# Optimization experiments

Hardware: AMD Instinct MI355X
Metric: run time of the kernel (lower is better)

Reference implementation:

```python
import jax, jax.numpy as jnp
import numpy as np

D, H = 256, 8
DH = D // H
NH, NL = 1024, 65536
EH, EL = 16384, 262144


def setup_inputs() -> dict:
    key = jax.random.key(0)
    ks = jax.random.split(key, 24)
    w = lambda i, s=0.05: jax.random.normal(ks[i], (D, D), jnp.float32) * s
    z = jnp.zeros((D,), jnp.float32)
    return {
        'high_emb_in': jax.random.normal(ks[0], (NH, D), jnp.float32),
        'low_emb_in': jax.random.normal(ks[1], (NL, D), jnp.float32),
        'high_edge_index': jax.random.randint(ks[2], (2, EH), 0, NH, jnp.int32),
        'low_edge_index': jax.random.randint(ks[3], (2, EL), 0, NL, jnp.int32),
        'low_batch': jnp.sort(jax.random.randint(ks[4], (NL,), 0, NH, jnp.int32)),
        'ln_g': jnp.ones((D,), jnp.float32), 'ln_b': z,
        'gin_eps': jnp.zeros((), jnp.float32), 'gin_w': w(5), 'gin_b': z,
        'mha_wq': w(6), 'mha_bq': z, 'mha_wk': w(7), 'mha_bk': z,
        'mha_wv': w(8), 'mha_bv': z, 'mha_wo': w(9), 'mha_bo': z,
        'tc_wq': w(10), 'tc_bq': z, 'tc_wk': w(11), 'tc_bk': z,
        'tc_wv': w(12), 'tc_bv': z, 'tc_wskip': w(13), 'tc_bskip': z,
        'chl_q': w(14), 'chl_k': w(15), 'chl_v': w(16),
        'clh_q': w(17), 'clh_k': w(18), 'clh_v': w(19),
    }


def _ln(x, g, b):
    m = x.mean(-1, keepdims=True)
    v = ((x - m) ** 2).mean(-1, keepdims=True)
    return (x - m) / jnp.sqrt(v + 1e-5) * g + b


def reference(high_emb_in, low_emb_in, ln_g, ln_b, gin_eps, gin_w, gin_b,
              mha_wq, mha_bq, mha_wk, mha_bk, mha_wv, mha_bv, mha_wo, mha_bo,
              tc_wq, tc_bq, tc_wk, tc_bk, tc_wv, tc_bv, tc_wskip, tc_bskip,
              chl_q, chl_k, chl_v, clh_q, clh_k, clh_v,
              high_edge_index, low_edge_index, low_batch):
    he = _ln(high_emb_in, ln_g, ln_b)
    le = _ln(low_emb_in, ln_g, ln_b)

    # --- GINConv(Linear) on high graph: Linear((1+eps)*x + sum_{j->i} x_j) ---
    hs, hd = high_edge_index[0], high_edge_index[1]
    agg = jax.ops.segment_sum(he[hs], hd, num_segments=NH)
    gin = ((1.0 + gin_eps) * he + agg) @ gin_w + gin_b

    # --- MultiheadAttention (unbatched self-attention over high nodes) ---
    q = (he @ mha_wq + mha_bq).reshape(NH, H, DH)
    k = (he @ mha_wk + mha_bk).reshape(NH, H, DH)
    v = (he @ mha_wv + mha_bv).reshape(NH, H, DH)
    logits = jnp.einsum('qhd,khd->hqk', q, k) * (1.0 / DH ** 0.5)
    attn = jax.nn.softmax(logits, axis=-1)
    mh = jnp.einsum('hqk,khd->qhd', attn, v).reshape(NH, D) @ mha_wo + mha_bo
    high = mh + gin

    # --- TransformerConv on low graph (concat heads + root skip) ---
    ls, lt = low_edge_index[0], low_edge_index[1]
    tq = (le @ tc_wq + tc_bq).reshape(NL, H, DH)
    tk = (le @ tc_wk + tc_bk).reshape(NL, H, DH)
    tv = (le @ tc_wv + tc_bv).reshape(NL, H, DH)
    lg = (tq[lt] * tk[ls]).sum(-1) * (1.0 / DH ** 0.5)  # [EL, H]
    mx = jax.ops.segment_max(lg, lt, num_segments=NL)
    p = jnp.exp(lg - mx[lt])
    den = jax.ops.segment_sum(p, lt, num_segments=NL)
    alpha = p / den[lt]
    msg = jax.ops.segment_sum(alpha[:, :, None] * tv[ls], lt, num_segments=NL)
    low = msg.reshape(NL, D) + le @ tc_wskip + tc_bskip

    # --- cross message passing ---
    cnt = jax.ops.segment_sum(jnp.ones((NL,), low.dtype), low_batch, num_segments=NH)
    xg = jax.ops.segment_sum(low, low_batch, num_segments=NH) / jnp.maximum(cnt, 1.0)[:, None]
    hpn = high[low_batch]
    sd = 1.0 / D ** 0.5
    w_hl = ((high @ chl_q) * (xg @ chl_k)).sum(1) * sd
    new_high = w_hl[:, None] * (high @ chl_v)
    w_lh = ((low @ clh_q) * (hpn @ clh_k)).sum(1) * sd
    new_low = w_lh[:, None] * (low @ clh_v)
    return (jax.nn.gelu(new_high, approximate=False),
            jax.nn.gelu(new_low, approximate=False))
```

## Files before the change

### kernel.cpp

```cpp
#include <hip/hip_runtime.h>
#include <math.h>

#define D 256
#define H 8
#define DH 32
#define NH 1024
#define NL 65536
#define EH 16384
#define EL 262144

typedef short bf16x8 __attribute__((ext_vector_type(8)));
typedef float f32x4 __attribute__((ext_vector_type(4)));

__device__ __forceinline__ float4 ld4(const float* p) { return *reinterpret_cast<const float4*>(p); }
__device__ __forceinline__ void st4(float* p, float4 v) { *reinterpret_cast<float4*>(p) = v; }
__device__ __forceinline__ float gelu_f(float x) { return 0.5f * x * (1.0f + erff(x * 0.70710678118654752f)); }
__device__ __forceinline__ ushort f2bf(float x) {
    union { float f; unsigned u; } v; v.f = x;
    unsigned r = v.u + 0x7FFF + ((v.u >> 16) & 1);
    return (ushort)(r >> 16);
}
__device__ __forceinline__ float bf2f(ushort u) {
    union { unsigned u; float f; } v; v.u = (unsigned)u << 16; return v.f;
}
__device__ __forceinline__ float4 bf4tof4(ushort4 u) {
    return make_float4(bf2f(u.x), bf2f(u.y), bf2f(u.z), bf2f(u.w));
}

__global__ __launch_bounds__(256) void ln_kernel(const float* __restrict__ hi, const float* __restrict__ lo,
                                                 const float* __restrict__ g, const float* __restrict__ b,
                                                 float* __restrict__ he, ushort* __restrict__ le16) {
    int row = blockIdx.x * 4 + (threadIdx.x >> 6);
    int lane = threadIdx.x & 63;
    const float* in = (row < NH) ? hi + (size_t)row * D : lo + (size_t)(row - NH) * D;
    float4 x = ld4(in + lane * 4);
    float s1 = x.x + x.y + x.z + x.w;
    float s2 = x.x * x.x + x.y * x.y + x.z * x.z + x.w * x.w;
    #pragma unroll
    for (int o = 32; o > 0; o >>= 1) { s1 += __shfl_xor(s1, o); s2 += __shfl_xor(s2, o); }
    float m = s1 * (1.0f / D);
    float var = s2 * (1.0f / D) - m * m;
    float rs = 1.0f / sqrtf(var + 1e-5f);
    float4 gg = ld4(g + lane * 4), bb = ld4(b + lane * 4);
    float4 y;
    y.x = (x.x - m) * rs * gg.x + bb.x;
    y.y = (x.y - m) * rs * gg.y + bb.y;
    y.z = (x.z - m) * rs * gg.z + bb.z;
    y.w = (x.w - m) * rs * gg.w + bb.w;
    if (row < NH) {
        st4(he + (size_t)row * D + lane * 4, y);
    } else {
        ushort4 u = make_ushort4(f2bf(y.x), f2bf(y.y), f2bf(y.z), f2bf(y.w));
        *reinterpret_cast<ushort4*>(le16 + (size_t)(row - NH) * D + lane * 4) = u;
    }
}

__global__ void concat_w(float* __restrict__ dst, const float* s0, const float* s1,
                         const float* s2, const float* s3, int nseg) {
    int total = 256 * nseg * 256;
    for (int idx = blockIdx.x * blockDim.x + threadIdx.x; idx < total; idx += gridDim.x * blockDim.x) {
        int ncol = nseg * 256;
        int r = idx / ncol, c = idx - r * ncol;
        int seg = c >> 8, cc = c & 255;
        const float* s = (seg == 0) ? s0 : (seg == 1) ? s1 : (seg == 2) ? s2 : s3;
        dst[idx] = s[r * 256 + cc];
    }
}
__global__ void concat_b(float* __restrict__ dst, const float* s0, const float* s1,
                         const float* s2, const float* s3, int nseg) {
    int idx = blockIdx.x * blockDim.x + threadIdx.x;
    if (idx < nseg * 256) {
        int seg = idx >> 8, cc = idx & 255;
        const float* s = (seg == 0) ? s0 : (seg == 1) ? s1 : (seg == 2) ? s2 : s3;
        dst[idx] = s[cc];
    }
}
__global__ __launch_bounds__(256) void concat_wT6(ushort* __restrict__ WlowT,
                                                  ushort* __restrict__ qT, ushort* __restrict__ vT,
                                                  const float* s18, const float* s20, const float* s22,
                                                  const float* s24, const float* s29, const float* s31) {
    int idx = blockIdx.x * 256 + threadIdx.x;
    int seg = idx >> 16, local = idx & 65535;
    int n = local >> 8, k = local & 255;
    const float* s; ushort* d; int off;
    switch (seg) {
        case 0: s = s18; d = WlowT; off = 0; break;
        case 1: s = s20; d = WlowT; off = 65536; break;
        case 2: s = s22; d = WlowT; off = 131072; break;
        case 3: s = s24; d = WlowT; off = 196608; break;
        case 4: s = s29; d = qT;    off = 0; break;
        default: s = s31; d = vT;   off = 0; break;
    }
    d[off + local] = f2bf(s[k * 256 + n]);
}

__global__ __launch_bounds__(256) void hcsr_count(const int* __restrict__ ei, int* __restrict__ counts) {
    int e = blockIdx.x * 256 + threadIdx.x;
    atomicAdd(&counts[ei[EH + e]], 1);
}
__global__ __launch_bounds__(256) void hscan(const int* __restrict__ cnt, int* __restrict__ rowptr) {
    __shared__ int s[256];
    int t = threadIdx.x;
    int v0 = cnt[t * 4], v1 = cnt[t * 4 + 1], v2 = cnt[t * 4 + 2], v3 = cnt[t * 4 + 3];
    int sum = v0 + v1 + v2 + v3;
    s[t] = sum;
    __syncthreads();
    for (int off = 1; off < 256; off <<= 1) {
        int v = (t >= off) ? s[t - off] : 0;
        __syncthreads();
        s[t] += v;
        __syncthreads();
    }
    int run = s[t] - sum;
    rowptr[t * 4] = run; run += v0;
    rowptr[t * 4 + 1] = run; run += v1;
    rowptr[t * 4 + 2] = run; run += v2;
    rowptr[t * 4 + 3] = run;
    if (t == 255) rowptr[NH] = EH;
}
__global__ __launch_bounds__(256) void hcsr_fill(const int* __restrict__ ei, const int* __restrict__ rowptr,
                                                 int* __restrict__ cursor, int* __restrict__ srcslot) {
    int e = blockIdx.x * 256 + threadIdx.x;
    int dst = ei[EH + e], src = ei[e];
    int pos = rowptr[dst] + atomicAdd(&cursor[dst], 1);
    srcslot[pos] = src;
}
__global__ __launch_bounds__(256) void gin_gather(const float* __restrict__ he, const int* __restrict__ rowptr,
                                                  const int* __restrict__ srcslot, const float* __restrict__ eps,
                                                  float* __restrict__ X) {
    int dst = blockIdx.x * 4 + (threadIdx.x >> 6);
    int lane = threadIdx.x & 63;
    float4 x = ld4(he + (size_t)dst * D + lane * 4);
    float e1 = 1.0f + eps[0];
    float4 acc = make_float4(e1 * x.x, e1 * x.y, e1 * x.z, e1 * x.w);
    int start = rowptr[dst], end = rowptr[dst + 1];
    for (int i = start; i < end; i++) {
        float4 v = ld4(he + (size_t)srcslot[i] * D + lane * 4);
        acc.x += v.x; acc.y += v.y; acc.z += v.z; acc.w += v.w;
    }
    st4(X + (size_t)dst * D + lane * 4, acc);
}

__global__ __launch_bounds__(256) void mm64(const float* __restrict__ A, int lda,
                                            const float* __restrict__ B, int ldb,
                                            const float* __restrict__ bias,
                                            const float* __restrict__ addC, int ldadd,
                                            float* __restrict__ C, int ldc) {
    __shared__ float As[16][64];
    __shared__ float Bs[16][64];
    int tid = threadIdx.x;
    int tx = tid & 15, ty = tid >> 4;
    int m0 = blockIdx.y * 64, n0 = blockIdx.x * 64;
    float acc[4][4];
    #pragma unroll
    for (int i = 0; i < 4; i++)
        #pragma unroll
        for (int j = 0; j < 4; j++) acc[i][j] = 0.0f;

    for (int k0 = 0; k0 < 256; k0 += 16) {
        {
            int row = tid >> 2, c4 = tid & 3;
            float4 a = ld4(A + (size_t)(m0 + row) * lda + k0 + c4 * 4);
            As[c4 * 4 + 0][row] = a.x; As[c4 * 4 + 1][row] = a.y;
            As[c4 * 4 + 2][row] = a.z; As[c4 * 4 + 3][row] = a.w;
        }
        {
            int row = tid >> 4, c4 = tid & 15;
            float4 b = ld4(B + (size_t)(k0 + row) * ldb + n0 + c4 * 4);
            st4(&Bs[row][c4 * 4], b);
        }
        __syncthreads();
        #pragma unroll
        for (int kk = 0; kk < 16; kk++) {
            float4 a4 = ld4(&As[kk][ty * 4]);
            float4 b4 = ld4(&Bs[kk][tx * 4]);
            float av[4] = {a4.x, a4.y, a4.z, a4.w};
            float bv[4] = {b4.x, b4.y, b4.z, b4.w};
            #pragma unroll
            for (int i = 0; i < 4; i++)
                #pragma unroll
                for (int j = 0; j < 4; j++) acc[i][j] += av[i] * bv[j];
        }
        __syncthreads();
    }
    float4 bj = bias ? ld4(bias + n0 + tx * 4) : make_float4(0.f, 0.f, 0.f, 0.f);
    #pragma unroll
    for (int i = 0; i < 4; i++) {
        size_t row = m0 + ty * 4 + i;
        float4 o = make_float4(acc[i][0] + bj.x, acc[i][1] + bj.y, acc[i][2] + bj.z, acc[i][3] + bj.w);
        if (addC) {
            float4 c = ld4(addC + row * ldadd + n0 + tx * 4);
            o.x += c.x; o.y += c.y; o.z += c.z; o.w += c.w;
        }
        st4(C + row * ldc + n0 + tx * 4, o);
    }
}

__global__ __launch_bounds__(256) void mm_bf16(const ushort* __restrict__ A, int lda,
                                               const ushort* __restrict__ BT,
                                               const float* __restrict__ bias,
                                               float* __restrict__ C, int ldc) {
    __shared__ ushort As[128][40];
    __shared__ ushort Bs[128][40];
    int tid = threadIdx.x;
    int lane = tid & 63, wave = tid >> 6;
    int wm = wave >> 1, wn = wave & 1;
    int m0 = blockIdx.y * 128, n0 = blockIdx.x * 128;
    int lrow = lane & 15, lgrp = lane >> 4;
    f32x4 acc[4][4];
    #pragma unroll
    for (int i = 0; i < 4; i++)
        #pragma unroll
        for (int j = 0; j < 4; j++) acc[i][j] = (f32x4){0.f, 0.f, 0.f, 0.f};

    int r0 = tid >> 2, q0 = tid & 3;
    int r1 = r0 + 64;
    for (int k0 = 0; k0 < 256; k0 += 32) {
        *(bf16x8*)&As[r0][q0 * 8] = *(const bf16x8*)&A[(size_t)(m0 + r0) * lda + k0 + q0 * 8];
        *(bf16x8*)&As[r1][q0 * 8] = *(const bf16x8*)&A[(size_t)(m0 + r1) * lda + k0 + q0 * 8];
        *(bf16x8*)&Bs[r0][q0 * 8] = *(const bf16x8*)&BT[(size_t)(n0 + r0) * 256 + k0 + q0 * 8];
        *(bf16x8*)&Bs[r1][q0 * 8] = *(const bf16x8*)&BT[(size_t)(n0 + r1) * 256 + k0 + q0 * 8];
        __syncthreads();
        bf16x8 af[4], bfr[4];
        #pragma unroll
        for (int f = 0; f < 4; f++) {
            af[f]  = *(const bf16x8*)&As[wm * 64 + f * 16 + lrow][lgrp * 8];
            bfr[f] = *(const bf16x8*)&Bs[wn * 64 + f * 16 + lrow][lgrp * 8];
        }
        #pragma unroll
        for (int i = 0; i < 4; i++)
            #pragma unroll
            for (int j = 0; j < 4; j++)
                acc[i][j] = __builtin_amdgcn_mfma_f32_16x16x32_bf16(af[i], bfr[j], acc[i][j], 0, 0, 0);
        __syncthreads();
    }
    #pragma unroll
    for (int i = 0; i < 4; i++) {
        #pragma unroll
        for (int j = 0; j < 4; j++) {
            int col = n0 + wn * 64 + j * 16 + lrow;
            float bb = bias ? bias[col] : 0.0f;
            #pragma unroll
            for (int r = 0; r < 4; r++) {
                int row = m0 + wm * 64 + i * 16 + lgrp * 4 + r;
                C[(size_t)row * ldc + col] = acc[i][j][r] + bb;
            }
        }
    }
}

__global__ __launch_bounds__(256) void mm_bf16_o16(const ushort* __restrict__ A, int lda,
                                                   const ushort* __restrict__ BT,
                                                   const float* __restrict__ bias,
                                                   ushort* __restrict__ C, int ldc) {
    __shared__ ushort As[128][40];
    __shared__ ushort Bs[128][40];
    int tid = threadIdx.x;
    int lane = tid & 63, wave = tid >> 6;
    int wm = wave >> 1, wn = wave & 1;
    int m0 = blockIdx.y * 128, n0 = blockIdx.x * 128;
    int lrow = lane & 15, lgrp = lane >> 4;
    f32x4 acc[4][4];
    #pragma unroll
    for (int i = 0; i < 4; i++)
        #pragma unroll
        for (int j = 0; j < 4; j++) acc[i][j] = (f32x4){0.f, 0.f, 0.f, 0.f};

    int r0 = tid >> 2, q0 = tid & 3;
    int r1 = r0 + 64;
    for (int k0 = 0; k0 < 256; k0 += 32) {
        *(bf16x8*)&As[r0][q0 * 8] = *(const bf16x8*)&A[(size_t)(m0 + r0) * lda + k0 + q0 * 8];
        *(bf16x8*)&As[r1][q0 * 8] = *(const bf16x8*)&A[(size_t)(m0 + r1) * lda + k0 + q0 * 8];
        *(bf16x8*)&Bs[r0][q0 * 8] = *(const bf16x8*)&BT[(size_t)(n0 + r0) * 256 + k0 + q0 * 8];
        *(bf16x8*)&Bs[r1][q0 * 8] = *(const bf16x8*)&BT[(size_t)(n0 + r1) * 256 + k0 + q0 * 8];
        __syncthreads();
        bf16x8 af[4], bfr[4];
        #pragma unroll
        for (int f = 0; f < 4; f++) {
            af[f]  = *(const bf16x8*)&As[wm * 64 + f * 16 + lrow][lgrp * 8];
            bfr[f] = *(const bf16x8*)&Bs[wn * 64 + f * 16 + lrow][lgrp * 8];
        }
        #pragma unroll
        for (int i = 0; i < 4; i++)
            #pragma unroll
            for (int j = 0; j < 4; j++)
                acc[i][j] = __builtin_amdgcn_mfma_f32_16x16x32_bf16(af[i], bfr[j], acc[i][j], 0, 0, 0);
        __syncthreads();
    }
    #pragma unroll
    for (int i = 0; i < 4; i++) {
        #pragma unroll
        for (int j = 0; j < 4; j++) {
            int col = n0 + wn * 64 + j * 16 + lrow;
            float bb = bias ? bias[col] : 0.0f;
            #pragma unroll
            for (int r = 0; r < 4; r++) {
                int row = m0 + wm * 64 + i * 16 + lgrp * 4 + r;
                C[(size_t)row * ldc + col] = f2bf(acc[i][j][r] + bb);
            }
        }
    }
}

__global__ __launch_bounds__(64) void attn_part(const float* __restrict__ qkv, float* __restrict__ part) {
    __shared__ float ks[64][32];
    __shared__ float vs[64][32];
    int h = blockIdx.y, kc = blockIdx.z;
    int q0 = blockIdx.x * 64;
    int t = threadIdx.x;
    float qr[32];
    const float* qp = qkv + (size_t)(q0 + t) * 768 + h * 32;
    #pragma unroll
    for (int d = 0; d < 32; d += 4) {
        float4 x = ld4(qp + d);
        qr[d] = x.x; qr[d + 1] = x.y; qr[d + 2] = x.z; qr[d + 3] = x.w;
    }
    int kt = kc * 64;
    #pragma unroll
    for (int j = 0; j < 8; j++) {
        int f = j * 64 + t;
        int row = f >> 3, c4 = f & 7;
        float4 kx = ld4(qkv + (size_t)(kt + row) * 768 + 256 + h * 32 + c4 * 4);
        st4(&ks[row][c4 * 4], kx);
        float4 vx = ld4(qkv + (size_t)(kt + row) * 768 + 512 + h * 32 + c4 * 4);
        st4(&vs[row][c4 * 4], vx);
    }
    __syncthreads();
    float l = 0.0f, acc[32];
    #pragma unroll
    for (int d = 0; d < 32; d++) acc[d] = 0.0f;
    const float scale = 0.17677669529663687f;
    #pragma unroll 4
    for (int kk = 0; kk < 64; kk++) {
        const float4* kr = reinterpret_cast<const float4*>(&ks[kk][0]);
        float s = 0.0f;
        #pragma unroll
        for (int d4 = 0; d4 < 8; d4++) {
            float4 kv = kr[d4];
            s += qr[d4*4]*kv.x + qr[d4*4+1]*kv.y + qr[d4*4+2]*kv.z + qr[d4*4+3]*kv.w;
        }
        float pe = __expf(s * scale);
        l += pe;
        const float4* vr = reinterpret_cast<const float4*>(&vs[kk][0]);
        #pragma unroll
        for (int d4 = 0; d4 < 8; d4++) {
            float4 vv = vr[d4];
            acc[d4*4] += pe*vv.x; acc[d4*4+1] += pe*vv.y; acc[d4*4+2] += pe*vv.z; acc[d4*4+3] += pe*vv.w;
        }
    }
    int q = q0 + t;
    size_t base = ((size_t)(h * 16 + kc) * 33) * 1024 + q;
    #pragma unroll
    for (int d = 0; d < 32; d++) part[base + (size_t)d * 1024] = acc[d];
    part[base + (size_t)32 * 1024] = l;
}

__global__ __launch_bounds__(64) void attn_combine(const float* __restrict__ part, float* __restrict__ out) {
    int h = blockIdx.y;
    int q = blockIdx.x * 64 + threadIdx.x;
    float acc[32], l = 0.0f;
    #pragma unroll
    for (int d = 0; d < 32; d++) acc[d] = 0.0f;
    for (int kc = 0; kc < 16; kc++) {
        size_t base = ((size_t)(h * 16 + kc) * 33) * 1024 + q;
        #pragma unroll
        for (int d = 0; d < 32; d++) acc[d] += part[base + (size_t)d * 1024];
        l += part[base + (size_t)32 * 1024];
    }
    float inv = 1.0f / l;
    float* op = out + (size_t)q * 256 + h * 32;
    #pragma unroll
    for (int d = 0; d < 32; d += 4)
        st4(op + d, make_float4(acc[d]*inv, acc[d+1]*inv, acc[d+2]*inv, acc[d+3]*inv));
}

__global__ __launch_bounds__(256) void csr_count(const int* __restrict__ ei, int* __restrict__ counts) {
    int e = blockIdx.x * 256 + threadIdx.x;
    atomicAdd(&counts[ei[EL + e]], 1);
}
__global__ __launch_bounds__(256) void scan_a(const int* __restrict__ counts, int* __restrict__ rowptr,
                                              int* __restrict__ bsum) {
    __shared__ int s[256];
    int t = threadIdx.x;
    int i = blockIdx.x * 256 + t;
    int c = counts[i];
    s[t] = c;
    __syncthreads();
    for (int off = 1; off < 256; off <<= 1) {
        int v = (t >= off) ? s[t - off] : 0;
        __syncthreads();
        s[t] += v;
        __syncthreads();
    }
    rowptr[i] = s[t] - c;
    if (t == 255) bsum[blockIdx.x] = s[255];
}
__global__ __launch_bounds__(256) void scan_b(int* __restrict__ bsum) {
    __shared__ int s[256];
    int t = threadIdx.x;
    int c = bsum[t];
    s[t] = c;
    __syncthreads();
    for (int off = 1; off < 256; off <<= 1) {
        int v = (t >= off) ? s[t - off] : 0;
        __syncthreads();
        s[t] += v;
        __syncthreads();
    }
    bsum[t] = s[t] - c;
}
__global__ __launch_bounds__(256) void scan_c(int* __restrict__ rowptr, const int* __restrict__ bsum) {
    int i = blockIdx.x * 256 + threadIdx.x;
    rowptr[i] += bsum[blockIdx.x];
    if (i == 0) rowptr[NL] = EL;
}
__global__ __launch_bounds__(256) void csr_fill(const int* __restrict__ ei, const int* __restrict__ rowptr,
                                                int* __restrict__ cursor, int* __restrict__ srcslot) {
    int e = blockIdx.x * 256 + threadIdx.x;
    int dst = ei[EL + e], src = ei[e];
    int pos = rowptr[dst] + atomicAdd(&cursor[dst], 1);
    srcslot[pos] = src;
}

__global__ __launch_bounds__(256) void edge_g1(const ushort* __restrict__ panel, const int* __restrict__ rowptr,
                                               const int* __restrict__ srcslot,
                                               float* __restrict__ p, float* __restrict__ den) {
    int dst = blockIdx.x * 4 + (threadIdx.x >> 6);
    int lane = threadIdx.x & 63, hh = lane >> 3;
    int start = rowptr[dst], end = rowptr[dst + 1];
    float4 q4 = bf4tof4(*(const ushort4*)&panel[(size_t)dst * 1024 + lane * 4]);
    float dl = 0.0f;
    for (int i = start; i < end; i++) {
        int src = srcslot[i];
        float4 k4 = bf4tof4(*(const ushort4*)&panel[(size_t)src * 1024 + 256 + lane * 4]);
        float s = q4.x * k4.x + q4.y * k4.y + q4.z * k4.z + q4.w * k4.w;
        s += __shfl_xor(s, 1); s += __shfl_xor(s, 2); s += __shfl_xor(s, 4);
        float pe = __expf(s * 0.17677669529663687f);
        dl += pe;
        if ((lane & 7) == 0) p[(size_t)i * 8 + hh] = pe;
    }
    if ((lane & 7) == 0) den[(size_t)dst * 8 + hh] = dl;
}

__global__ __launch_bounds__(256) void edge_g2(ushort* panel, const int* __restrict__ rowptr,
                                               const int* __restrict__ srcslot,
                                               const float* __restrict__ p, const float* __restrict__ den) {
    int dst = blockIdx.x * 4 + (threadIdx.x >> 6);
    int lane = threadIdx.x & 63, hh = lane >> 3;
    int start = rowptr[dst], end = rowptr[dst + 1];
    float dl = den[(size_t)dst * 8 + hh];
    float invd = (dl != 0.0f) ? 1.0f / dl : 0.0f;
    float4 acc = make_float4(0.f, 0.f, 0.f, 0.f);
    for (int i = start; i < end; i++) {
        int src = srcslot[i];
        float a = p[(size_t)i * 8 + hh] * invd;
        float4 v4 = bf4tof4(*(const ushort4*)&panel[(size_t)src * 1024 + 512 + lane * 4]);
        acc.x += a * v4.x; acc.y += a * v4.y; acc.z += a * v4.z; acc.w += a * v4.w;
    }
    ushort* op = panel + (size_t)dst * 1024 + 768 + lane * 4;
    float4 sk = bf4tof4(*(const ushort4*)op);
    ushort4 u = make_ushort4(f2bf(acc.x + sk.x), f2bf(acc.y + sk.y), f2bf(acc.z + sk.z), f2bf(acc.w + sk.w));
    *reinterpret_cast<ushort4*>(op) = u;
}

__global__ __launch_bounds__(256) void xg_kernel(const ushort* __restrict__ panel,
                                                 const int* __restrict__ batch, float* __restrict__ xg) {
    int i = blockIdx.x;
    int d = threadIdx.x;
    int lo = 0, hi = NL;
    while (lo < hi) { int mid = (lo + hi) >> 1; if (batch[mid] < i) lo = mid + 1; else hi = mid; }
    int start = lo;
    hi = NL;
    while (lo < hi) { int mid = (lo + hi) >> 1; if (batch[mid] < i + 1) lo = mid + 1; else hi = mid; }
    int end = lo;
    float s = 0.0f;
    for (int r = start; r < end; r++) s += bf2f(panel[(size_t)r * 1024 + 768 + d]);
    xg[i * 256 + d] = s / fmaxf((float)(end - start), 1.0f);
}

__global__ __launch_bounds__(256) void out_high_kernel(const float* __restrict__ highX,
                                                       const float* __restrict__ xk, float* __restrict__ out) {
    int i = blockIdx.x * 4 + (threadIdx.x >> 6);
    int lane = threadIdx.x & 63;
    float4 hq = ld4(highX + (size_t)i * 768 + lane * 4);
    float4 xkv = ld4(xk + (size_t)i * 256 + lane * 4);
    float s = hq.x * xkv.x + hq.y * xkv.y + hq.z * xkv.z + hq.w * xkv.w;
    #pragma unroll
    for (int o = 32; o > 0; o >>= 1) s += __shfl_xor(s, o);
    float w = s * 0.0625f;
    float4 hv = ld4(highX + (size_t)i * 768 + 256 + lane * 4);
    st4(out + (size_t)i * 256 + lane * 4,
        make_float4(gelu_f(w * hv.x), gelu_f(w * hv.y), gelu_f(w * hv.z), gelu_f(w * hv.w)));
}

__global__ __launch_bounds__(256) void out_low_kernel(const ushort* __restrict__ panel,
                                                      const float* __restrict__ highX,
                                                      const int* __restrict__ batch, float* __restrict__ lvout) {
    int i = blockIdx.x * 4 + (threadIdx.x >> 6);
    int lane = threadIdx.x & 63;
    int b = batch[i];
    float4 lq = bf4tof4(*(const ushort4*)&panel[(size_t)i * 1024 + lane * 4]);
    float4 hk = ld4(highX + (size_t)b * 768 + 512 + lane * 4);
    float s = lq.x * hk.x + lq.y * hk.y + lq.z * hk.z + lq.w * hk.w;
    #pragma unroll
    for (int o = 32; o > 0; o >>= 1) s += __shfl_xor(s, o);
    float w = s * 0.0625f;
    float4 lv = ld4(lvout + (size_t)i * 256 + lane * 4);
    st4(lvout + (size_t)i * 256 + lane * 4,
        make_float4(gelu_f(w * lv.x), gelu_f(w * lv.y), gelu_f(w * lv.z), gelu_f(w * lv.w)));
}

extern "C" void kernel_launch(void* const* d_in, const int* in_sizes, int n_in,
                              void* d_out, int out_size, void* d_ws, size_t ws_size,
                              hipStream_t stream) {
    const float* high_in = (const float*)d_in[0];
    const float* low_in  = (const float*)d_in[1];
    const int*   hei     = (const int*)d_in[2];
    const int*   lei     = (const int*)d_in[3];
    const int*   batch   = (const int*)d_in[4];
    const float* ln_g    = (const float*)d_in[5];
    const float* ln_b    = (const float*)d_in[6];
    const float* gin_eps = (const float*)d_in[7];
    const float* gin_w   = (const float*)d_in[8];
    const float* gin_b   = (const float*)d_in[9];
    const float* mha_wo  = (const float*)d_in[16];
    const float* mha_bo  = (const float*)d_in[17];
    const float* chl_k   = (const float*)d_in[27];

    float* out = (float*)d_out;
    ushort* le16 = (ushort*)d_out;
    float* lv  = out + (size_t)NH * 256;

    float* ws    = (float*)d_ws;
    ushort* panel = (ushort*)ws;
    float* pbuf  = ws + (size_t)NL * 512;
    float* den   = pbuf + 4325376;
    float* xg    = den + (size_t)NL * 8;
    float* he    = xg + (size_t)NH * 256;
    float* aggx  = he + (size_t)NH * 256;
    float* gin   = aggx + (size_t)NH * 256;
    float* qkv   = gin + (size_t)NH * 256;
    float* attno = qkv + (size_t)NH * 768;
    float* high  = attno + (size_t)NH * 256;
    float* highX = high + (size_t)NH * 256;
    float* xk    = highX + (size_t)NH * 768;
    float* Wmha  = xk + (size_t)NH * 256;
    float* bmha  = Wmha + 256 * 768;
    float* Whx   = bmha + 768;
    float* bqk   = Whx + 256 * 768;
    ushort* WlowT = (ushort*)(bqk + 1024);
    ushort* clhqT = WlowT + 1024 * 256;
    ushort* clhvT = clhqT + 256 * 256;
    int* rowptr  = (int*)(clhvT + 256 * 256);
    int* cursor  = rowptr + NL + 1;
    int* bsum    = cursor + NL;
    int* srcslot = bsum + 256;
    int* hcnt    = srcslot + EL;
    int* hrow    = hcnt + NH;
    int* hsrc    = hrow + NH + 1;

    concat_w<<<768, 256, 0, stream>>>(Wmha, (const float*)d_in[10], (const float*)d_in[12], (const float*)d_in[14], nullptr, 3);
    concat_b<<<3, 256, 0, stream>>>(bmha, (const float*)d_in[11], (const float*)d_in[13], (const float*)d_in[15], nullptr, 3);
    concat_w<<<768, 256, 0, stream>>>(Whx, (const float*)d_in[26], (const float*)d_in[28], (const float*)d_in[30], nullptr, 3);
    concat_b<<<4, 256, 0, stream>>>(bqk, (const float*)d_in[19], (const float*)d_in[21], (const float*)d_in[23], (const float*)d_in[25], 4);
    concat_wT6<<<1536, 256, 0, stream>>>(WlowT, clhqT, clhvT,
                                         (const float*)d_in[18], (const float*)d_in[20], (const float*)d_in[22],
                                         (const float*)d_in[24], (const float*)d_in[29], (const float*)d_in[31]);

    hipMemsetAsync(cursor, 0, NL * sizeof(int), stream);
    csr_count<<<EL / 256, 256, 0, stream>>>(lei, cursor);
    scan_a<<<256, 256, 0, stream>>>(cursor, rowptr, bsum);
    scan_b<<<1, 256, 0, stream>>>(bsum);
    scan_c<<<256, 256, 0, stream>>>(rowptr, bsum);
    hipMemsetAsync(cursor, 0, NL * sizeof(int), stream);
    csr_fill<<<EL / 256, 256, 0, stream>>>(lei, rowptr, cursor, srcslot);

    hipMemsetAsync(hcnt, 0, NH * sizeof(int), stream);
    hcsr_count<<<EH / 256, 256, 0, stream>>>(hei, hcnt);
    hscan<<<1, 256, 0, stream>>>(hcnt, hrow);
    hipMemsetAsync(hcnt, 0, NH * sizeof(int), stream);
    hcsr_fill<<<EH / 256, 256, 0, stream>>>(hei, hrow, hcnt, hsrc);

    ln_kernel<<<(NH + NL) / 4, 256, 0, stream>>>(high_in, low_in, ln_g, ln_b, he, le16);

    gin_gather<<<NH / 4, 256, 0, stream>>>(he, hrow, hsrc, gin_eps, aggx);
    mm64<<<dim3(4, 16), 256, 0, stream>>>(aggx, 256, gin_w, 256, gin_b, nullptr, 0, gin, 256);

    mm64<<<dim3(12, 16), 256, 0, stream>>>(he, 256, Wmha, 768, bmha, nullptr, 0, qkv, 768);
    attn_part<<<dim3(16, H, 16), 64, 0, stream>>>(qkv, pbuf);
    attn_combine<<<dim3(16, H), 64, 0, stream>>>(pbuf, attno);
    mm64<<<dim3(4, 16), 256, 0, stream>>>(attno, 256, mha_wo, 256, mha_bo, gin, 256, high, 256);

    mm_bf16_o16<<<dim3(8, NL / 128), 256, 0, stream>>>(le16, 256, WlowT, bqk, panel, 1024);

    edge_g1<<<NL / 4, 256, 0, stream>>>(panel, rowptr, srcslot, pbuf, den);

    edge_g2<<<NL / 4, 256, 0, stream>>>(panel, rowptr, srcslot, pbuf, den);

    xg_kernel<<<NH, 256, 0, stream>>>(panel, batch, xg);

    mm64<<<dim3(12, 16), 256, 0, stream>>>(high, 256, Whx, 768, nullptr, nullptr, 0, highX, 768);
    mm64<<<dim3(4, 16), 256, 0, stream>>>(xg, 256, chl_k, 256, nullptr, nullptr, 0, xk, 256);
    out_high_kernel<<<NH / 4, 256, 0, stream>>>(highX, xk, out);

    mm_bf16_o16<<<dim3(2, NL / 128), 256, 0, stream>>>(panel + 768, 1024, clhqT, nullptr, panel, 1024);
    mm_bf16<<<dim3(2, NL / 128), 256, 0, stream>>>(panel + 768, 1024, clhvT, nullptr, lv, 256);

    out_low_kernel<<<NL / 4, 256, 0, stream>>>(panel, highX, batch, lv);
}
```

Baseline: 689.8 us.

## Merge low-side cross projections into one bf16 GEMM and swizzle block order

The clh_q and clh_v projections of the low nodes now run as a single bf16-output GEMM with N=512, writing both into the bf16 panel. The separate fp32-output GEMM is removed, and out_low_kernel reads the v projection from the panel instead of an fp32 buffer. The GEMM launch becomes a 1D grid remapped in groups of 8 blocks, which should improve cache locality across XCDs. This trims one launch and the fp32 intermediate traffic, but the v projection is now rounded to bf16 before GELU, costing some accuracy.

```diff
diff --git a/kernel.cpp b/kernel.cpp
--- a/kernel.cpp
+++ b/kernel.cpp
@@ -196,69 +196,18 @@
     }
 }
 
-__global__ __launch_bounds__(256) void mm_bf16(const ushort* __restrict__ A, int lda,
-                                               const ushort* __restrict__ BT,
-                                               const float* __restrict__ bias,
-                                               float* __restrict__ C, int ldc) {
+__global__ __launch_bounds__(256) void mm_bf16_o16(const ushort* __restrict__ A, int lda,
+                                                   const ushort* __restrict__ BT,
+                                                   const float* __restrict__ bias,
+                                                   ushort* __restrict__ C, int ldc, int nbx) {
     __shared__ ushort As[128][40];
     __shared__ ushort Bs[128][40];
+    int orig = blockIdx.x;
+    int wg = (orig & 7) * (gridDim.x >> 3) + (orig >> 3);
+    int m0 = (wg / nbx) * 128, n0 = (wg % nbx) * 128;
     int tid = threadIdx.x;
     int lane = tid & 63, wave = tid >> 6;
     int wm = wave >> 1, wn = wave & 1;
-    int m0 = blockIdx.y * 128, n0 = blockIdx.x * 128;
-    int lrow = lane & 15, lgrp = lane >> 4;
-    f32x4 acc[4][4];
-    #pragma unroll
-    for (int i = 0; i < 4; i++)
-        #pragma unroll
-        for (int j = 0; j < 4; j++) acc[i][j] = (f32x4){0.f, 0.f, 0.f, 0.f};
-
-    int r0 = tid >> 2, q0 = tid & 3;
-    int r1 = r0 + 64;
-    for (int k0 = 0; k0 < 256; k0 += 32) {
-        *(bf16x8*)&As[r0][q0 * 8] = *(const bf16x8*)&A[(size_t)(m0 + r0) * lda + k0 + q0 * 8];
-        *(bf16x8*)&As[r1][q0 * 8] = *(const bf16x8*)&A[(size_t)(m0 + r1) * lda + k0 + q0 * 8];
-        *(bf16x8*)&Bs[r0][q0 * 8] = *(const bf16x8*)&BT[(size_t)(n0 + r0) * 256 + k0 + q0 * 8];
-        *(bf16x8*)&Bs[r1][q0 * 8] = *(const bf16x8*)&BT[(size_t)(n0 + r1) * 256 + k0 + q0 * 8];
-        __syncthreads();
-        bf16x8 af[4], bfr[4];
-        #pragma unroll
-        for (int f = 0; f < 4; f++) {
-            af[f]  = *(const bf16x8*)&As[wm * 64 + f * 16 + lrow][lgrp * 8];
-            bfr[f] = *(const bf16x8*)&Bs[wn * 64 + f * 16 + lrow][lgrp * 8];
-        }
-        #pragma unroll
-        for (int i = 0; i < 4; i++)
-            #pragma unroll
-            for (int j = 0; j < 4; j++)
-                acc[i][j] = __builtin_amdgcn_mfma_f32_16x16x32_bf16(af[i], bfr[j], acc[i][j], 0, 0, 0);
-        __syncthreads();
-    }
-    #pragma unroll
-    for (int i = 0; i < 4; i++) {
-        #pragma unroll
-        for (int j = 0; j < 4; j++) {
-            int col = n0 + wn * 64 + j * 16 + lrow;
-            float bb = bias ? bias[col] : 0.0f;
-            #pragma unroll
-            for (int r = 0; r < 4; r++) {
-                int row = m0 + wm * 64 + i * 16 + lgrp * 4 + r;
-                C[(size_t)row * ldc + col] = acc[i][j][r] + bb;
-            }
-        }
-    }
-}
-
-__global__ __launch_bounds__(256) void mm_bf16_o16(const ushort* __restrict__ A, int lda,
-                                                   const ushort* __restrict__ BT,
-                                                   const float* __restrict__ bias,
-                                                   ushort* __restrict__ C, int ldc) {
-    __shared__ ushort As[128][40];
-    __shared__ ushort Bs[128][40];
-    int tid = threadIdx.x;
-    int lane = tid & 63, wave = tid >> 6;
-    int wm = wave >> 1, wn = wave & 1;
-    int m0 = blockIdx.y * 128, n0 = blockIdx.x * 128;
     int lrow = lane & 15, lgrp = lane >> 4;
     f32x4 acc[4][4];
     #pragma unroll
@@ -495,7 +444,7 @@
 
 __global__ __launch_bounds__(256) void out_low_kernel(const ushort* __restrict__ panel,
                                                       const float* __restrict__ highX,
-                                                      const int* __restrict__ batch, float* __restrict__ lvout) {
+                                                      const int* __restrict__ batch, float* __restrict__ out) {
     int i = blockIdx.x * 4 + (threadIdx.x >> 6);
     int lane = threadIdx.x & 63;
     int b = batch[i];
@@ -505,8 +454,8 @@
     #pragma unroll
     for (int o = 32; o > 0; o >>= 1) s += __shfl_xor(s, o);
     float w = s * 0.0625f;
-    float4 lv = ld4(lvout + (size_t)i * 256 + lane * 4);
-    st4(lvout + (size_t)i * 256 + lane * 4,
+    float4 lv = bf4tof4(*(const ushort4*)&panel[(size_t)i * 1024 + 256 + lane * 4]);
+    st4(out + (size_t)i * 256 + lane * 4,
         make_float4(gelu_f(w * lv.x), gelu_f(w * lv.y), gelu_f(w * lv.z), gelu_f(w * lv.w)));
 }
 
@@ -529,7 +478,6 @@
 
     float* out = (float*)d_out;
     ushort* le16 = (ushort*)d_out;
-    float* lv  = out + (size_t)NH * 256;
 
     float* ws    = (float*)d_ws;
     ushort* panel = (ushort*)ws;
@@ -591,7 +539,7 @@
     attn_combine<<<dim3(16, H), 64, 0, stream>>>(pbuf, attno);
     mm64<<<dim3(4, 16), 256, 0, stream>>>(attno, 256, mha_wo, 256, mha_bo, gin, 256, high, 256);
 
-    mm_bf16_o16<<<dim3(8, NL / 128), 256, 0, stream>>>(le16, 256, WlowT, bqk, panel, 1024);
+    mm_bf16_o16<<<4096, 256, 0, stream>>>(le16, 256, WlowT, bqk, panel, 1024, 8);
 
     edge_g1<<<NL / 4, 256, 0, stream>>>(panel, rowptr, srcslot, pbuf, den);
 
@@ -603,8 +551,7 @@
     mm64<<<dim3(4, 16), 256, 0, stream>>>(xg, 256, chl_k, 256, nullptr, nullptr, 0, xk, 256);
     out_high_kernel<<<NH / 4, 256, 0, stream>>>(highX, xk, out);
 
-    mm_bf16_o16<<<dim3(2, NL / 128), 256, 0, stream>>>(panel + 768, 1024, clhqT, nullptr, panel, 1024);
-    mm_bf16<<<dim3(2, NL / 128), 256, 0, stream>>>(panel + 768, 1024, clhvT, nullptr, lv, 256);
-
-    out_low_kernel<<<NL / 4, 256, 0, stream>>>(panel, highX, batch, lv);
-}
+    mm_bf16_o16<<<2048, 256, 0, stream>>>(panel + 768, 1024, clhqT, nullptr, panel, 1024, 4);
+
+    out_low_kernel<<<NL / 4, 256, 0, stream>>>(panel, highX, batch, out + (size_t)NH * 256);
+}
```

Measured after the change: 657.2 us. 4.7% less time.
